# Optimization experiments

Hardware: AMD Instinct MI355X
Metric: run time of the kernel (lower is better)

The kernel has to match this reference:

```python
import jax, jax.numpy as jnp
import numpy as np

N = 100000      # nodes
E = 1600000     # edges
F_IN = 256      # num_features
H = 128         # hidden_dim
C = 16          # num_classes
LOG_SIGMA0 = float(np.log(0.1))  # prior_sigma = 0.1


def setup_inputs() -> dict:
    key = jax.random.key(0)
    ks = jax.random.split(key, 8)
    x = jax.random.normal(ks[0], (N, F_IN), jnp.float32)
    edge_index = jax.random.randint(ks[1], (2, E), 0, N, dtype=jnp.int64)
    # GCNConv linear weight + bias
    W = jax.random.normal(ks[2], (F_IN, H), jnp.float32) / np.float32(np.sqrt(F_IN))
    gcn_b = jnp.zeros((H,), jnp.float32)
    # BayesLinear params (mu + log_sigma) and fixed sampled noise eps
    w_mu = jax.random.normal(ks[3], (C, H), jnp.float32) / np.float32(np.sqrt(H))
    w_log_sigma = jnp.full((C, H), LOG_SIGMA0, jnp.float32)
    b_mu = jnp.zeros((C,), jnp.float32)
    b_log_sigma = jnp.full((C,), LOG_SIGMA0, jnp.float32)
    eps_w = jax.random.normal(ks[4], (C, H), jnp.float32)
    eps_b = jax.random.normal(ks[5], (C,), jnp.float32)
    return {"x": x, "edge_index": edge_index, "W": W, "gcn_b": gcn_b,
            "w_mu": w_mu, "w_log_sigma": w_log_sigma,
            "b_mu": b_mu, "b_log_sigma": b_log_sigma,
            "eps_w": eps_w, "eps_b": eps_b}


def reference(x, edge_index, W, gcn_b, w_mu, w_log_sigma, b_mu, b_log_sigma, eps_w, eps_b):
    n = x.shape[0]
    # --- GCNConv: add self-loops, symmetric deg^{-1/2} normalization ---
    loop = jnp.arange(n, dtype=edge_index.dtype)
    src = jnp.concatenate([edge_index[0], loop])  # message source j
    dst = jnp.concatenate([edge_index[1], loop])  # aggregation target i
    deg = jax.ops.segment_sum(jnp.ones_like(dst, dtype=x.dtype), dst, num_segments=n)
    deg_inv_sqrt = jnp.where(deg > 0, jax.lax.rsqrt(deg), 0.0)
    norm = deg_inv_sqrt[src] * deg_inv_sqrt[dst]            # [E+N]
    h = x @ W                                               # [N,H] transform first
    msg = h[src] * norm[:, None]                            # [E+N,H] gather
    agg = jax.ops.segment_sum(msg, dst, num_segments=n)     # [N,H] scatter-add
    agg = agg + gcn_b
    # --- ReLU; dropout is identity in eval mode ---
    a = jax.nn.relu(agg)
    # --- BayesLinear: w = mu + exp(log_sigma) * eps ---
    w = w_mu + jnp.exp(w_log_sigma) * eps_w                 # [C,H]
    b = b_mu + jnp.exp(b_log_sigma) * eps_b                 # [C]
    logits = a @ w.T + b                                    # [N,C]
    return jax.nn.log_softmax(logits, axis=1)
```

## Files before the change

### kernel.cpp

```cpp
#include <hip/hip_runtime.h>
#include <hip/hip_bf16.h>

#define N_NODES 100000
#define F_IN    256
#define H_DIM   128
#define C_CLS   16
#define NB_SCAN ((N_NODES + 255) / 256)
#define NSHARD  8
#define SHARD_W ((N_NODES + NSHARD - 1) / NSHARD)

typedef __attribute__((ext_vector_type(8))) short  short8;
typedef __attribute__((ext_vector_type(4))) float  float4v;
typedef __attribute__((ext_vector_type(4))) unsigned short ushort4v;

__device__ __forceinline__ float b2f(ushort u) {
    union { unsigned int i; float f; } v;
    v.i = ((unsigned int)u) << 16;
    return v.f;
}

__device__ __forceinline__ ushort f2b(float f) {
    unsigned int x = __float_as_uint(f);
    unsigned int r = (x + 0x7FFFu + ((x >> 16) & 1u)) >> 16;
    return (ushort)r;
}

__device__ __forceinline__ float ldsel(const void* p, int i, int f32f) {
    return f32f ? ((const float*)p)[i] : b2f(((const ushort*)p)[i]);
}

__global__ __launch_bounds__(64) void sniff(const ushort* __restrict__ x,
                                            const int* __restrict__ ei,
                                            int* __restrict__ flags) {
    int lane = threadIdx.x;
    int cnt_bf = 0;
#pragma unroll
    for (int j = 0; j < 4; ++j) {
        ushort u = x[lane * 4 + j];
        int e = (u >> 7) & 0xFF;
        if ((e >= 100 && e <= 140) || (u & 0x7FFF) == 0) cnt_bf++;
    }
    int zodd = (ei[2 * lane + 1] == 0) ? 1 : 0;
#pragma unroll
    for (int off = 32; off >= 1; off >>= 1) {
        cnt_bf += __shfl_xor(cnt_bf, off, 64);
        zodd   += __shfl_xor(zodd,   off, 64);
    }
    if (lane == 0) {
        flags[0] = (cnt_bf < 230) ? 1 : 0;
        flags[1] = (zodd  >= 32) ? 1 : 0;
    }
}

__global__ __launch_bounds__(256) void prep_params(const int* __restrict__ flags,
                                                   const void* __restrict__ W_any,
                                                   ushort* __restrict__ wtg,
                                                   const void* __restrict__ w_mu,
                                                   const void* __restrict__ w_ls,
                                                   const void* __restrict__ eps_w,
                                                   const void* __restrict__ b_mu,
                                                   const void* __restrict__ b_ls,
                                                   const void* __restrict__ eps_b,
                                                   const void* __restrict__ gcn_b,
                                                   ushort* __restrict__ whi,
                                                   ushort* __restrict__ wlo,
                                                   float* __restrict__ bias16,
                                                   float* __restrict__ gcnb_f) {
    const int f32f = flags[0];
    const int t = threadIdx.x;
    if (blockIdx.x < H_DIM) {
        const int n = blockIdx.x;
        float v = f32f ? ((const float*)W_any)[t * H_DIM + n]
                       : b2f(((const ushort*)W_any)[t * H_DIM + n]);
        wtg[n * F_IN + t] = f2b(v);
        return;
    }
#pragma unroll
    for (int i = t; i < C_CLS * H_DIM; i += 256) {
        float v = ldsel(w_mu, i, f32f) + __expf(ldsel(w_ls, i, f32f)) * ldsel(eps_w, i, f32f);
        ushort h = f2b(v);
        whi[i] = h;
        wlo[i] = f2b(v - b2f(h));
    }
    if (t < C_CLS)
        bias16[t] = ldsel(b_mu, t, f32f) + __expf(ldsel(b_ls, t, f32f)) * ldsel(eps_b, t, f32f);
    if (t < H_DIM)
        gcnb_f[t] = ldsel(gcn_b, t, f32f);
}

__global__ __launch_bounds__(256) void prep(const int* __restrict__ flags,
                                            const int* __restrict__ ei,
                                            int* __restrict__ cnt,
                                            int2* __restrict__ pr, int E) {
    int e = blockIdx.x * 256 + threadIdx.x;
    if (e >= E) return;
    int i64 = flags[1];
    int s = i64 ? ei[2L * e]          : ei[e];
    int d = i64 ? ei[2L * E + 2L * e] : ei[(long)E + e];
    pr[e] = make_int2(s, d);
    atomicAdd(&cnt[d], 1);
}

__global__ __launch_bounds__(256) void scan1(const int* __restrict__ cnt,
                                             int* __restrict__ offs,
                                             int* __restrict__ bsum) {
    __shared__ int sd[256];
    int t = threadIdx.x;
    int i = blockIdx.x * 256 + t;
    int v = (i < N_NODES) ? cnt[i] : 0;
    sd[t] = v;
    __syncthreads();
#pragma unroll
    for (int d = 1; d < 256; d <<= 1) {
        int add = (t >= d) ? sd[t - d] : 0;
        __syncthreads();
        sd[t] += add;
        __syncthreads();
    }
    if (i < N_NODES) offs[i] = sd[t] - v;
    if (t == 255) bsum[blockIdx.x] = sd[255];
}

__global__ __launch_bounds__(512) void scan2(const int* __restrict__ bsum,
                                             int* __restrict__ boff) {
    __shared__ int sd[512];
    int t = threadIdx.x;
    int v = (t < NB_SCAN) ? bsum[t] : 0;
    sd[t] = v;
    __syncthreads();
#pragma unroll
    for (int d = 1; d < 512; d <<= 1) {
        int add = (t >= d) ? sd[t - d] : 0;
        __syncthreads();
        sd[t] += add;
        __syncthreads();
    }
    if (t < NB_SCAN) boff[t] = sd[t] - v;
}

__global__ __launch_bounds__(256) void scan3(int* __restrict__ offs,
                                             const int* __restrict__ boff,
                                             const int* __restrict__ cnt,
                                             int* __restrict__ cursor,
                                             float* __restrict__ dis, int E) {
    int i = blockIdx.x * 256 + threadIdx.x;
    if (i == 0) offs[N_NODES] = E;
    if (i >= N_NODES) return;
    int off = offs[i] + boff[i >> 8];
    offs[i] = off;
    cursor[i] = off;
    dis[i] = rsqrtf((float)(cnt[i] + 1));
}

__global__ __launch_bounds__(256) void build_perm(const int2* __restrict__ pr,
                                                  int* __restrict__ cursor,
                                                  int* __restrict__ perm, int E) {
    const int shard = blockIdx.x & (NSHARD - 1);
    const int jb    = blockIdx.x >> 3;
    const int nb    = gridDim.x >> 3;
    const int lo = shard * SHARD_W;
    const int hi = lo + SHARD_W;
    for (int e = jb * 256 + threadIdx.x; e < E; e += nb * 256) {
        int2 p = pr[e];
        if (p.y >= lo && p.y < hi) {
            int slot = atomicAdd(&cursor[p.y], 1);
            perm[slot] = p.x;
        }
    }
}

__global__ __launch_bounds__(256) void gemm_xw(const int* __restrict__ flags,
                                               const void* __restrict__ x_any,
                                               const ushort* __restrict__ wtg,
                                               const float* __restrict__ dis,
                                               ushort* __restrict__ hout) {
    __shared__ __align__(16) ushort wt[128 * 128];
    const int f32f = flags[0];

    const int tid  = threadIdx.x;
    const int lane = tid & 63;
    const int quad = lane >> 4;
    const int lm   = lane & 15;
    const int wave = tid >> 6;

    const int rbase = blockIdx.x * 128 + wave * 32;
    int arow0 = rbase + lm;
    int arow1 = rbase + 16 + lm;
    if (arow0 >= N_NODES) arow0 = N_NODES - 1;
    if (arow1 >= N_NODES) arow1 = N_NODES - 1;
    const float*  xrf0 = (const float*) x_any + (size_t)arow0 * F_IN;
    const float*  xrf1 = (const float*) x_any + (size_t)arow1 * F_IN;
    const ushort* xrb0 = (const ushort*)x_any + (size_t)arow0 * F_IN;
    const ushort* xrb1 = (const ushort*)x_any + (size_t)arow1 * F_IN;

    float4v acc0[8], acc1[8];
#pragma unroll
    for (int c = 0; c < 8; ++c) {
        acc0[c] = (float4v){0.f, 0.f, 0.f, 0.f};
        acc1[c] = (float4v){0.f, 0.f, 0.f, 0.f};
    }

    for (int hh = 0; hh < 2; ++hh) {
        if (hh) __syncthreads();
#pragma unroll
        for (int it = 0; it < 8; ++it) {
            int flat = (it * 256 + tid) * 8;
            int col  = flat >> 7;
            int kloc = flat & 127;
            short8 v = *(const short8*)(wtg + col * F_IN + hh * 128 + kloc);
            int dst = ((col << 7) | kloc) ^ ((col & 7) << 3);
            *(short8*)(wt + dst) = v;
        }
        __syncthreads();
#pragma unroll
        for (int s = 0; s < 4; ++s) {
            int klocal = s * 32 + quad * 8;
            short8 afrag0, afrag1;
            if (f32f) {
                const float* p0 = xrf0 + hh * 128 + klocal;
                const float* p1 = xrf1 + hh * 128 + klocal;
                float4 u0 = *(const float4*)p0;
                float4 u1 = *(const float4*)(p0 + 4);
                float4 u2 = *(const float4*)p1;
                float4 u3 = *(const float4*)(p1 + 4);
                afrag0[0] = (short)f2b(u0.x); afrag0[1] = (short)f2b(u0.y);
                afrag0[2] = (short)f2b(u0.z); afrag0[3] = (short)f2b(u0.w);
                afrag0[4] = (short)f2b(u1.x); afrag0[5] = (short)f2b(u1.y);
                afrag0[6] = (short)f2b(u1.z); afrag0[7] = (short)f2b(u1.w);
                afrag1[0] = (short)f2b(u2.x); afrag1[1] = (short)f2b(u2.y);
                afrag1[2] = (short)f2b(u2.z); afrag1[3] = (short)f2b(u2.w);
                afrag1[4] = (short)f2b(u3.x); afrag1[5] = (short)f2b(u3.y);
                afrag1[6] = (short)f2b(u3.z); afrag1[7] = (short)f2b(u3.w);
            } else {
                afrag0 = *(const short8*)(xrb0 + hh * 128 + klocal);
                afrag1 = *(const short8*)(xrb1 + hh * 128 + klocal);
            }
#pragma unroll
            for (int c = 0; c < 8; ++c) {
                int colr = c * 16 + lm;
                int src = ((colr << 7) | klocal) ^ ((lm & 7) << 3);
                short8 bfrag = *(const short8*)(wt + src);
                acc0[c] = __builtin_amdgcn_mfma_f32_16x16x32_bf16(afrag0, bfrag, acc0[c], 0, 0, 0);
                acc1[c] = __builtin_amdgcn_mfma_f32_16x16x32_bf16(afrag1, bfrag, acc1[c], 0, 0, 0);
            }
        }
    }
    float dv0[4], dv1[4];
#pragma unroll
    for (int r = 0; r < 4; ++r) {
        int n0 = rbase + quad * 4 + r;
        int n1 = rbase + 16 + quad * 4 + r;
        dv0[r] = (n0 < N_NODES) ? dis[n0] : 0.f;
        dv1[r] = (n1 < N_NODES) ? dis[n1] : 0.f;
    }
#pragma unroll
    for (int c = 0; c < 8; ++c) {
        int col = c * 16 + lm;
#pragma unroll
        for (int r = 0; r < 4; ++r) {
            int n0 = rbase + quad * 4 + r;
            int n1 = rbase + 16 + quad * 4 + r;
            if (n0 < N_NODES) hout[(size_t)n0 * H_DIM + col] = f2b(acc0[c][r] * dv0[r]);
            if (n1 < N_NODES) hout[(size_t)n1 * H_DIM + col] = f2b(acc1[c][r] * dv1[r]);
        }
    }
}

__global__ __launch_bounds__(256) void gather_final(const int* __restrict__ flags,
                                                    const int* __restrict__ offs,
                                                    const int* __restrict__ perm,
                                                    const float* __restrict__ dis,
                                                    const ushort* __restrict__ hb,
                                                    const float* __restrict__ gcnb_f,
                                                    const ushort* __restrict__ whi,
                                                    const ushort* __restrict__ wlo,
                                                    const float* __restrict__ bias16,
                                                    void* __restrict__ out) {
    __shared__ __align__(16) ushort alds[16][136];
    const int f32f = flags[0];
    const int lane = threadIdx.x & 63;
    const int wave = threadIdx.x >> 6;
    const int n0 = blockIdx.x * 16;

    for (int r = 0; r < 4; ++r) {
        const int node = n0 + wave * 4 + r;
        const int off0 = __builtin_amdgcn_readfirstlane(offs[node]);
        const int deg  = __builtin_amdgcn_readfirstlane(offs[node + 1]) - off0;
        const int* pp = perm + off0;

        float ax = 0.f, ay = 0.f;
        const int full = deg & ~15;
        for (int base = 0; base < full; base += 16) {
#pragma unroll
            for (int k = 0; k < 16; ++k) {
                int sk = pp[base + k];
                uint u = *((const uint*)(hb + (size_t)sk * H_DIM) + lane);
                ax += __uint_as_float(u << 16);
                ay += __uint_as_float(u & 0xFFFF0000u);
            }
        }
        {
            const int nb = deg - full;
#pragma unroll
            for (int k = 0; k < 16; ++k) {
                int   sk = 0;
                float wk = 0.f;
                if (k < nb) { sk = pp[full + k]; wk = 1.f; }
                uint u = *((const uint*)(hb + (size_t)sk * H_DIM) + lane);
                ax = fmaf(wk, __uint_as_float(u << 16),         ax);
                ay = fmaf(wk, __uint_as_float(u & 0xFFFF0000u), ay);
            }
        }

        const float dd = dis[node];
        uint us = *((const uint*)(hb + (size_t)node * H_DIM) + lane);
        float2 gb = *(const float2*)(gcnb_f + 2 * lane);
        ax = (ax + __uint_as_float(us << 16))         * dd + gb.x;
        ay = (ay + __uint_as_float(us & 0xFFFF0000u)) * dd + gb.y;
        ax = fmaxf(ax, 0.f);
        ay = fmaxf(ay, 0.f);
        uint pack = (uint)f2b(ax) | ((uint)f2b(ay) << 16);
        *((uint*)&alds[wave * 4 + r][2 * lane]) = pack;
    }
    __syncthreads();
    if (wave != 0) return;

    const int lm = lane & 15, quad = lane >> 4;
    const ushort* bh = whi + lm * H_DIM + quad * 8;
    const ushort* bl = wlo + lm * H_DIM + quad * 8;

    float4v acc = (float4v){0.f, 0.f, 0.f, 0.f};
#pragma unroll
    for (int s = 0; s < 4; ++s) {
        short8 af = *(const short8*)&alds[lm][quad * 8 + s * 32];
        short8 b0 = *(const short8*)(bh + s * 32);
        short8 b1 = *(const short8*)(bl + s * 32);
        acc = __builtin_amdgcn_mfma_f32_16x16x32_bf16(af, b0, acc, 0, 0, 0);
        acc = __builtin_amdgcn_mfma_f32_16x16x32_bf16(af, b1, acc, 0, 0, 0);
    }

    const float bias = bias16[lm];
    float p[4], m[4], ss[4];
#pragma unroll
    for (int r = 0; r < 4; ++r) { p[r] = acc[r] + bias; m[r] = p[r]; }
#pragma unroll
    for (int off = 1; off < 16; off <<= 1)
#pragma unroll
        for (int r = 0; r < 4; ++r) m[r] = fmaxf(m[r], __shfl_xor(m[r], off, 64));
#pragma unroll
    for (int r = 0; r < 4; ++r) ss[r] = __expf(p[r] - m[r]);
#pragma unroll
    for (int off = 1; off < 16; off <<= 1)
#pragma unroll
        for (int r = 0; r < 4; ++r) ss[r] += __shfl_xor(ss[r], off, 64);

    if (f32f) {
        float* op = (float*)out;
#pragma unroll
        for (int r = 0; r < 4; ++r)
            op[(size_t)(n0 + quad * 4 + r) * C_CLS + lm] = p[r] - m[r] - __logf(ss[r]);
    } else {
        ushort* op = (ushort*)out;
#pragma unroll
        for (int r = 0; r < 4; ++r)
            op[(size_t)(n0 + quad * 4 + r) * C_CLS + lm] = f2b(p[r] - m[r] - __logf(ss[r]));
    }
}

extern "C" void kernel_launch(void* const* d_in, const int* in_sizes, int n_in,
                              void* d_out, int out_size, void* d_ws, size_t ws_size,
                              hipStream_t stream) {
    const int E = in_sizes[1] / 2;

    char* wp = (char*)d_ws;
    auto alloc = [&](size_t bytes) -> char* {
        char* p = wp; wp += (bytes + 511) & ~(size_t)511; return p;
    };
    int*    flags  = (int*)   alloc(64);
    ushort* hb     = (ushort*)alloc((size_t)N_NODES * H_DIM * 2);
    int*    cnt    = (int*)   alloc((size_t)N_NODES * 4);
    int*    offs   = (int*)   alloc((size_t)(N_NODES + 1) * 4);
    int*    cursor = (int*)   alloc((size_t)N_NODES * 4);
    int*    bsum   = (int*)   alloc((size_t)NB_SCAN * 4);
    int*    boff   = (int*)   alloc((size_t)NB_SCAN * 4);
    float*  dis    = (float*) alloc((size_t)N_NODES * 4);
    int*    perm   = (int*)   alloc((size_t)E * 4);
    int2*   pr     = (int2*)  alloc((size_t)E * 8);
    ushort* wtg    = (ushort*)alloc((size_t)H_DIM * F_IN * 2);
    ushort* whi    = (ushort*)alloc((size_t)C_CLS * H_DIM * 2);
    ushort* wlo    = (ushort*)alloc((size_t)C_CLS * H_DIM * 2);
    float*  bias16 = (float*) alloc((size_t)C_CLS * 4);
    float*  gcnb_f = (float*) alloc((size_t)H_DIM * 4);

    sniff<<<1, 64, 0, stream>>>((const ushort*)d_in[0], (const int*)d_in[1], flags);
    prep_params<<<H_DIM + 1, 256, 0, stream>>>(flags, d_in[2], wtg,
                                  d_in[4], d_in[5], d_in[8],
                                  d_in[6], d_in[7], d_in[9], d_in[3],
                                  whi, wlo, bias16, gcnb_f);
    (void)hipMemsetAsync(cnt, 0, (size_t)N_NODES * 4, stream);
    prep<<<(E + 255) / 256, 256, 0, stream>>>(flags, (const int*)d_in[1], cnt, pr, E);
    scan1<<<NB_SCAN, 256, 0, stream>>>(cnt, offs, bsum);
    scan2<<<1, 512, 0, stream>>>(bsum, boff);
    scan3<<<NB_SCAN, 256, 0, stream>>>(offs, boff, cnt, cursor, dis, E);
    build_perm<<<2048, 256, 0, stream>>>(pr, cursor, perm, E);
    gemm_xw<<<(N_NODES + 127) / 128, 256, 0, stream>>>(flags, d_in[0], wtg, dis, hb);
    gather_final<<<N_NODES / 16, 256, 0, stream>>>(flags, offs, perm, dis, hb,
                                                   gcnb_f, whi, wlo, bias16, (void*)d_out);
}
```

Baseline: 405.1 us.

## Record per-edge rank at count time and fuse scan stages and memset

The counting kernel now stores the value returned by each per-destination atomic increment as an edge rank, so the CSR fill can compute slots directly as offset plus rank and no longer needs the second pass of cursor atomics. The single-block second scan and the offset-adding third scan are merged into one kernel in which each block sums the preceding block totals itself. The memset of the count array moves into extra blocks of the parameter-prep kernel. These changes remove two launches and one round of atomics, at the cost of an extra E-sized rank array written and then read, and redundant prefix summing across blocks.

```diff
diff --git a/kernel.cpp b/kernel.cpp
--- a/kernel.cpp
+++ b/kernel.cpp
@@ -8,6 +8,7 @@
 #define NB_SCAN ((N_NODES + 255) / 256)
 #define NSHARD  8
 #define SHARD_W ((N_NODES + NSHARD - 1) / NSHARD)
+#define ZB      98
 
 typedef __attribute__((ext_vector_type(8))) short  short8;
 typedef __attribute__((ext_vector_type(4))) float  float4v;
@@ -65,7 +66,8 @@
                                                    ushort* __restrict__ whi,
                                                    ushort* __restrict__ wlo,
                                                    float* __restrict__ bias16,
-                                                   float* __restrict__ gcnb_f) {
+                                                   float* __restrict__ gcnb_f,
+                                                   int* __restrict__ cnt) {
     const int f32f = flags[0];
     const int t = threadIdx.x;
     if (blockIdx.x < H_DIM) {
@@ -75,6 +77,11 @@
         wtg[n * F_IN + t] = f2b(v);
         return;
     }
+    if (blockIdx.x > H_DIM) {
+        int idx4 = (blockIdx.x - H_DIM - 1) * 256 + t;
+        if (idx4 < N_NODES / 4) ((int4*)cnt)[idx4] = make_int4(0, 0, 0, 0);
+        return;
+    }
 #pragma unroll
     for (int i = t; i < C_CLS * H_DIM; i += 256) {
         float v = ldsel(w_mu, i, f32f) + __expf(ldsel(w_ls, i, f32f)) * ldsel(eps_w, i, f32f);
@@ -91,14 +98,15 @@
 __global__ __launch_bounds__(256) void prep(const int* __restrict__ flags,
                                             const int* __restrict__ ei,
                                             int* __restrict__ cnt,
-                                            int2* __restrict__ pr, int E) {
+                                            int2* __restrict__ pr,
+                                            int* __restrict__ rk, int E) {
     int e = blockIdx.x * 256 + threadIdx.x;
     if (e >= E) return;
     int i64 = flags[1];
     int s = i64 ? ei[2L * e]          : ei[e];
     int d = i64 ? ei[2L * E + 2L * e] : ei[(long)E + e];
     pr[e] = make_int2(s, d);
-    atomicAdd(&cnt[d], 1);
+    rk[e] = atomicAdd(&cnt[d], 1);
 }
 
 __global__ __launch_bounds__(256) void scan1(const int* __restrict__ cnt,
@@ -121,39 +129,34 @@
     if (t == 255) bsum[blockIdx.x] = sd[255];
 }
 
-__global__ __launch_bounds__(512) void scan2(const int* __restrict__ bsum,
-                                             int* __restrict__ boff) {
-    __shared__ int sd[512];
-    int t = threadIdx.x;
-    int v = (t < NB_SCAN) ? bsum[t] : 0;
-    sd[t] = v;
+__global__ __launch_bounds__(256) void scan23(int* __restrict__ offs,
+                                              const int* __restrict__ bsum,
+                                              const int* __restrict__ cnt,
+                                              float* __restrict__ dis, int E) {
+    __shared__ int ws[4];
+    const int t = threadIdx.x;
+    const int bid = blockIdx.x;
+    const int lane = t & 63;
+    const int wave = t >> 6;
+
+    int acc = 0;
+    for (int j = t; j < bid; j += 256) acc += bsum[j];
+#pragma unroll
+    for (int off = 32; off >= 1; off >>= 1) acc += __shfl_xor(acc, off, 64);
+    if (lane == 0) ws[wave] = acc;
     __syncthreads();
-#pragma unroll
-    for (int d = 1; d < 512; d <<= 1) {
-        int add = (t >= d) ? sd[t - d] : 0;
-        __syncthreads();
-        sd[t] += add;
-        __syncthreads();
-    }
-    if (t < NB_SCAN) boff[t] = sd[t] - v;
-}
-
-__global__ __launch_bounds__(256) void scan3(int* __restrict__ offs,
-                                             const int* __restrict__ boff,
-                                             const int* __restrict__ cnt,
-                                             int* __restrict__ cursor,
-                                             float* __restrict__ dis, int E) {
-    int i = blockIdx.x * 256 + threadIdx.x;
+    const int boffb = ws[0] + ws[1] + ws[2] + ws[3];
+
+    int i = bid * 256 + t;
     if (i == 0) offs[N_NODES] = E;
     if (i >= N_NODES) return;
-    int off = offs[i] + boff[i >> 8];
-    offs[i] = off;
-    cursor[i] = off;
+    offs[i] += boffb;
     dis[i] = rsqrtf((float)(cnt[i] + 1));
 }
 
 __global__ __launch_bounds__(256) void build_perm(const int2* __restrict__ pr,
-                                                  int* __restrict__ cursor,
+                                                  const int* __restrict__ rk,
+                                                  const int* __restrict__ offs,
                                                   int* __restrict__ perm, int E) {
     const int shard = blockIdx.x & (NSHARD - 1);
     const int jb    = blockIdx.x >> 3;
@@ -162,10 +165,8 @@
     const int hi = lo + SHARD_W;
     for (int e = jb * 256 + threadIdx.x; e < E; e += nb * 256) {
         int2 p = pr[e];
-        if (p.y >= lo && p.y < hi) {
-            int slot = atomicAdd(&cursor[p.y], 1);
-            perm[slot] = p.x;
-        }
+        if (p.y >= lo && p.y < hi)
+            perm[offs[p.y] + rk[e]] = p.x;
     }
 }
 
@@ -380,12 +381,11 @@
     ushort* hb     = (ushort*)alloc((size_t)N_NODES * H_DIM * 2);
     int*    cnt    = (int*)   alloc((size_t)N_NODES * 4);
     int*    offs   = (int*)   alloc((size_t)(N_NODES + 1) * 4);
-    int*    cursor = (int*)   alloc((size_t)N_NODES * 4);
     int*    bsum   = (int*)   alloc((size_t)NB_SCAN * 4);
-    int*    boff   = (int*)   alloc((size_t)NB_SCAN * 4);
     float*  dis    = (float*) alloc((size_t)N_NODES * 4);
     int*    perm   = (int*)   alloc((size_t)E * 4);
     int2*   pr     = (int2*)  alloc((size_t)E * 8);
+    int*    rk     = (int*)   alloc((size_t)E * 4);
     ushort* wtg    = (ushort*)alloc((size_t)H_DIM * F_IN * 2);
     ushort* whi    = (ushort*)alloc((size_t)C_CLS * H_DIM * 2);
     ushort* wlo    = (ushort*)alloc((size_t)C_CLS * H_DIM * 2);
@@ -393,16 +393,14 @@
     float*  gcnb_f = (float*) alloc((size_t)H_DIM * 4);
 
     sniff<<<1, 64, 0, stream>>>((const ushort*)d_in[0], (const int*)d_in[1], flags);
-    prep_params<<<H_DIM + 1, 256, 0, stream>>>(flags, d_in[2], wtg,
+    prep_params<<<H_DIM + 1 + ZB, 256, 0, stream>>>(flags, d_in[2], wtg,
                                   d_in[4], d_in[5], d_in[8],
                                   d_in[6], d_in[7], d_in[9], d_in[3],
-                                  whi, wlo, bias16, gcnb_f);
-    (void)hipMemsetAsync(cnt, 0, (size_t)N_NODES * 4, stream);
-    prep<<<(E + 255) / 256, 256, 0, stream>>>(flags, (const int*)d_in[1], cnt, pr, E);
+                                  whi, wlo, bias16, gcnb_f, cnt);
+    prep<<<(E + 255) / 256, 256, 0, stream>>>(flags, (const int*)d_in[1], cnt, pr, rk, E);
     scan1<<<NB_SCAN, 256, 0, stream>>>(cnt, offs, bsum);
-    scan2<<<1, 512, 0, stream>>>(bsum, boff);
-    scan3<<<NB_SCAN, 256, 0, stream>>>(offs, boff, cnt, cursor, dis, E);
-    build_perm<<<2048, 256, 0, stream>>>(pr, cursor, perm, E);
+    scan23<<<NB_SCAN, 256, 0, stream>>>(offs, bsum, cnt, dis, E);
+    build_perm<<<2048, 256, 0, stream>>>(pr, rk, offs, perm, E);
     gemm_xw<<<(N_NODES + 127) / 128, 256, 0, stream>>>(flags, d_in[0], wtg, dis, hb);
     gather_final<<<N_NODES / 16, 256, 0, stream>>>(flags, offs, perm, dis, hb,
                                                    gcnb_f, whi, wlo, bias16, (void*)d_out);
```

New measurement: 376.2 us. 1.08x faster.
